# Performance work log

Measured on AMD Instinct MI355X. Metric: run time of the kernel, lower is better.

## Reference

```python
import jax, jax.numpy as jnp
import numpy as np

SAMPLE_RATE = 16000
FREQ_LOW = 200.0
FREQ_HIGH = 1200.0
# deterministic stand-in for random.uniform(freq_low, freq_high): midpoint
FREQUENCY = 0.5 * (FREQ_LOW + FREQ_HIGH)  # 700 Hz
CUTOFF = FREQUENCY / SAMPLE_RATE          # normalized cutoff, as in cutoff_frequency()
Q = 0.70710678  # standard Butterworth-like quality factor for biquad highpass


def _biquad_highpass_coeffs(cutoff, q):
    # standard audio-EQ-cookbook highpass biquad, cutoff normalized to sample rate
    w0 = 2.0 * np.pi * cutoff
    cw, sw = np.cos(w0), np.sin(w0)
    alpha = sw / (2.0 * q)
    b0 = (1.0 + cw) / 2.0
    b1 = -(1.0 + cw)
    b2 = (1.0 + cw) / 2.0
    a0 = 1.0 + alpha
    a1 = -2.0 * cw
    a2 = 1.0 - alpha
    return (np.float32(b0 / a0), np.float32(b1 / a0), np.float32(b2 / a0),
            np.float32(a1 / a0), np.float32(a2 / a0))


def setup_inputs() -> dict:
    key = jax.random.key(0)
    B, C, T = 128, 2, 65536
    audio = jax.random.normal(key, (B, C, T), dtype=jnp.float32)
    return {"audio": audio}


def reference(audio) -> jnp.ndarray:
    b0, b1, b2, a1, a2 = _biquad_highpass_coeffs(CUTOFF, Q)
    x_t = jnp.moveaxis(audio, -1, 0)  # [T, B, C] for scan over time
    zero = jnp.zeros(x_t.shape[1:], dtype=audio.dtype)

    def step(carry, x):
        x1, x2, y1, y2 = carry
        # IIR biquad difference equation
        y = b0 * x + b1 * x1 + b2 * x2 - a1 * y1 - a2 * y2
        return (x, x1, y, y1), y

    _, y_t = jax.lax.scan(step, (zero, zero, zero, zero), x_t)
    return jnp.moveaxis(y_t, 0, -1)  # [B, C, T]
```

## Files before the change

### kernel.cpp

```cpp
#include <hip/hip_runtime.h>
#include <math.h>


#define T_LEN    65536
#define L_CHUNK  64
#define W_WARM   64
#define TS       32
#define BLK      64
#define ROWS     64
#define BUF_F    (ROWS * TS)
#define BLOCKS_PER_CH 16

#define WAITVM(n) asm volatile("s_waitcnt vmcnt(" #n ")" ::: "memory")

__device__ __forceinline__ void lds_fence() {
    asm volatile("s_waitcnt lgkmcnt(0)" ::: "memory");
}

__device__ __forceinline__ void dma_tile(const float* __restrict__ x,
                                         int base_f, int tile, float* buf)
{
    #pragma unroll
    for (int i = 0; i < 8; ++i) {
        int pos = base_f + i * 512 + tile * TS;
        pos = pos < 0 ? 0 : pos;
        __builtin_amdgcn_global_load_lds(
            (__attribute__((address_space(1))) void*)(void*)(x + pos),
            (__attribute__((address_space(3))) void*)(buf + i * 256),
            16, 0, 0);
    }
}

template <bool WARM>
__device__ __forceinline__ void tile_filter(float* buf, int lane, bool ch0,
    float c_b0, float c_b1, float c_b2, float c_a1, float c_a2,
    float& x1, float& x2, float& y1, float& y2)
{
    float4 r[8];
    #pragma unroll
    for (int g = 0; g < 8; ++g)
        r[g] = *(float4*)&buf[(lane * 8 + ((g + lane) & 7)) * 4];

    if (WARM && ch0) {
        #pragma unroll
        for (int g = 0; g < 8; ++g) r[g] = make_float4(0.f, 0.f, 0.f, 0.f);
    }

    #pragma unroll
    for (int g = 0; g < 8; ++g) {
        float4 v = r[g];
        float yv;
        yv = c_b0*v.x + c_b1*x1 + c_b2*x2 - c_a1*y1 - c_a2*y2;
        x2 = x1; x1 = v.x; y2 = y1; y1 = yv; v.x = yv;
        yv = c_b0*v.y + c_b1*x1 + c_b2*x2 - c_a1*y1 - c_a2*y2;
        x2 = x1; x1 = v.y; y2 = y1; y1 = yv; v.y = yv;
        yv = c_b0*v.z + c_b1*x1 + c_b2*x2 - c_a1*y1 - c_a2*y2;
        x2 = x1; x1 = v.z; y2 = y1; y1 = yv; v.z = yv;
        yv = c_b0*v.w + c_b1*x1 + c_b2*x2 - c_a1*y1 - c_a2*y2;
        x2 = x1; x1 = v.w; y2 = y1; y1 = yv; v.w = yv;
        if (!WARM) r[g] = v;
    }

    if (!WARM) {
        #pragma unroll
        for (int g = 0; g < 8; ++g)
            *(float4*)&buf[(lane * 8 + ((g + lane) & 7)) * 4] = r[g];
    }
}

__global__ __launch_bounds__(BLK, 4)
void hp_biquad_kernel(const float* __restrict__ x, float* __restrict__ y,
                      float c_b0, float c_b1, float c_b2, float c_a1, float c_a2)
{
    __shared__ float bufA[BUF_F];
    __shared__ float bufB[BUF_F];
    const int lane = threadIdx.x;
    const int cg0  = blockIdx.x * ROWS;
    const bool ch0 = ((blockIdx.x & (BLOCKS_PER_CH - 1)) == 0) && (lane == 0);

    const int l0  = lane >> 3;
    const int j0  = ((lane & 7) - l0) & 7;
    const int bsf = (cg0 + l0) * L_CHUNK - W_WARM + j0 * 4;

    float x1 = 0.f, x2 = 0.f, y1 = 0.f, y2 = 0.f;

    dma_tile(x, bsf, 0, bufA);
    dma_tile(x, bsf, 1, bufB);

    WAITVM(8);
    tile_filter<true>(bufA, lane, ch0, c_b0, c_b1, c_b2, c_a1, c_a2, x1, x2, y1, y2);
    lds_fence();
    dma_tile(x, bsf, 2, bufA);

    WAITVM(8);
    tile_filter<true>(bufB, lane, ch0, c_b0, c_b1, c_b2, c_a1, c_a2, x1, x2, y1, y2);
    lds_fence();
    dma_tile(x, bsf, 3, bufB);

    WAITVM(8);
    tile_filter<false>(bufA, lane, ch0, c_b0, c_b1, c_b2, c_a1, c_a2, x1, x2, y1, y2);

    WAITVM(0);
    tile_filter<false>(bufB, lane, ch0, c_b0, c_b1, c_b2, c_a1, c_a2, x1, x2, y1, y2);
    lds_fence();

    const int ybase = cg0 * L_CHUNK + lane * 4;
    #pragma unroll
    for (int p = 0; p < 16; ++p) {
        int q   = lane + p * 64;
        int seg = q >> 4;
        int jj  = q & 15;
        float* b = (jj < 8) ? bufA : bufB;
        int g   = jj & 7;
        float4 v = *(float4*)&b[(seg * 8 + ((g + seg) & 7)) * 4];
        *(float4*)(y + ybase + p * 256) = v;
    }
}

extern "C" void kernel_launch(void* const* d_in, const int* in_sizes, int n_in,
                              void* d_out, int out_size, void* d_ws, size_t ws_size,
                              hipStream_t stream)
{
    const float* x = (const float*)d_in[0];
    float* y = (float*)d_out;

    const double SR = 16000.0, FLO = 200.0, FHI = 1200.0;
    const double freq   = 0.5 * (FLO + FHI);
    const double cutoff = freq / SR;
    const double q      = 0.70710678;
    const double w0 = 2.0 * M_PI * cutoff;
    const double cw = cos(w0), sw = sin(w0);
    const double alpha = sw / (2.0 * q);
    const double b0 = (1.0 + cw) / 2.0;
    const double b1 = -(1.0 + cw);
    const double b2 = (1.0 + cw) / 2.0;
    const double a0 = 1.0 + alpha;
    const double a1 = -2.0 * cw;
    const double a2 = 1.0 - alpha;
    const float fb0 = (float)(b0 / a0), fb1 = (float)(b1 / a0), fb2 = (float)(b2 / a0);
    const float fa1 = (float)(a1 / a0), fa2 = (float)(a2 / a0);

    const int total  = 128 * 2 * T_LEN;
    const int chunks = total / L_CHUNK;
    const int blocks = chunks / ROWS;

    hp_biquad_kernel<<<blocks, BLK, 0, stream>>>(x, y, fb0, fb1, fb2, fa1, fa2);
    (void)in_sizes; (void)n_in; (void)out_size; (void)d_ws; (void)ws_size;
}
```

Measured before the change: 114.9 us.

## Lengthen per-thread chunks to amortize IIR warm-up with a streaming tile loop

New measurement: 137.7 us. +19.8%, slower.

```diff
diff --git a/kernel.cpp b/kernel.cpp
--- a/kernel.cpp
+++ b/kernel.cpp
@@ -3,13 +3,15 @@
 
 
 #define T_LEN    65536
-#define L_CHUNK  64
+#define L_CHUNK  256
 #define W_WARM   64
 #define TS       32
 #define BLK      64
 #define ROWS     64
 #define BUF_F    (ROWS * TS)
-#define BLOCKS_PER_CH 16
+#define BLOCKS_PER_CH ((T_LEN / L_CHUNK) / ROWS)
+#define N_TILES  ((L_CHUNK + W_WARM) / TS)
+#define N_PAIRS  ((N_TILES - 2) / 2)
 
 #define WAITVM(n) asm volatile("s_waitcnt vmcnt(" #n ")" ::: "memory")
 
@@ -22,7 +24,7 @@
 {
     #pragma unroll
     for (int i = 0; i < 8; ++i) {
-        int pos = base_f + i * 512 + tile * TS;
+        int pos = base_f + i * (8 * L_CHUNK) + tile * TS;
         pos = pos < 0 ? 0 : pos;
         __builtin_amdgcn_global_load_lds(
             (__attribute__((address_space(1))) void*)(void*)(x + pos),
@@ -68,7 +70,7 @@
     }
 }
 
-__global__ __launch_bounds__(BLK, 4)
+__global__ __launch_bounds__(BLK, 2)
 void hp_biquad_kernel(const float* __restrict__ x, float* __restrict__ y,
                       float c_b0, float c_b1, float c_b2, float c_a1, float c_a2)
 {
@@ -97,23 +99,39 @@
     lds_fence();
     dma_tile(x, bsf, 3, bufB);
 
-    WAITVM(8);
-    tile_filter<false>(bufA, lane, ch0, c_b0, c_b1, c_b2, c_a1, c_a2, x1, x2, y1, y2);
+    const int ybase = cg0 * L_CHUNK;
+    #pragma unroll
+    for (int p = 0; p < N_PAIRS; ++p) {
+        if (p == 0) { WAITVM(8); } else { WAITVM(24); }
+        tile_filter<false>(bufA, lane, ch0, c_b0, c_b1, c_b2, c_a1, c_a2, x1, x2, y1, y2);
+        if (p == 0) { WAITVM(0); } else { WAITVM(16); }
+        tile_filter<false>(bufB, lane, ch0, c_b0, c_b1, c_b2, c_a1, c_a2, x1, x2, y1, y2);
+        lds_fence();
 
-    WAITVM(0);
-    tile_filter<false>(bufB, lane, ch0, c_b0, c_b1, c_b2, c_a1, c_a2, x1, x2, y1, y2);
-    lds_fence();
+        float4 v[16];
+        #pragma unroll
+        for (int k = 0; k < 16; ++k) {
+            int q  = lane + k * 64;
+            int sg = q >> 4;
+            int jj = q & 15;
+            float* b = (jj < 8) ? bufA : bufB;
+            int g  = jj & 7;
+            v[k] = *(float4*)&b[(sg * 8 + ((g + sg) & 7)) * 4];
+        }
+        lds_fence();
 
-    const int ybase = cg0 * L_CHUNK + lane * 4;
-    #pragma unroll
-    for (int p = 0; p < 16; ++p) {
-        int q   = lane + p * 64;
-        int seg = q >> 4;
-        int jj  = q & 15;
-        float* b = (jj < 8) ? bufA : bufB;
-        int g   = jj & 7;
-        float4 v = *(float4*)&b[(seg * 8 + ((g + seg) & 7)) * 4];
-        *(float4*)(y + ybase + p * 256) = v;
+        if (p < N_PAIRS - 1) {
+            dma_tile(x, bsf, 2 * p + 4, bufA);
+            dma_tile(x, bsf, 2 * p + 5, bufB);
+        }
+
+        #pragma unroll
+        for (int k = 0; k < 16; ++k) {
+            int q  = lane + k * 64;
+            int sg = q >> 4;
+            int jj = q & 15;
+            *(float4*)(y + ybase + sg * L_CHUNK + p * 64 + jj * 4) = v[k];
+        }
     }
 }
 
```

## Halve chunk length to double parallelism with six-tile warmup pipeline

Applied to the files above, without the earlier changes.

Result: slower. 237.8 us (+106.9%).

```diff
diff --git a/kernel.cpp b/kernel.cpp
--- a/kernel.cpp
+++ b/kernel.cpp
@@ -3,13 +3,14 @@
 
 
 #define T_LEN    65536
-#define L_CHUNK  64
+#define L_CHUNK  32
 #define W_WARM   64
-#define TS       32
+#define TS       16
 #define BLK      64
 #define ROWS     64
 #define BUF_F    (ROWS * TS)
-#define BLOCKS_PER_CH 16
+#define BLOCKS_PER_CH ((T_LEN / L_CHUNK) / ROWS)
+#define N_TILES  ((L_CHUNK + W_WARM) / TS)
 
 #define WAITVM(n) asm volatile("s_waitcnt vmcnt(" #n ")" ::: "memory")
 
@@ -21,7 +22,7 @@
                                          int base_f, int tile, float* buf)
 {
     #pragma unroll
-    for (int i = 0; i < 8; ++i) {
+    for (int i = 0; i < 4; ++i) {
         int pos = base_f + i * 512 + tile * TS;
         pos = pos < 0 ? 0 : pos;
         __builtin_amdgcn_global_load_lds(
@@ -32,22 +33,22 @@
 }
 
 template <bool WARM>
-__device__ __forceinline__ void tile_filter(float* buf, int lane, bool ch0,
+__device__ __forceinline__ void tile_filter(float* buf, int lane, bool zr,
     float c_b0, float c_b1, float c_b2, float c_a1, float c_a2,
     float& x1, float& x2, float& y1, float& y2)
 {
-    float4 r[8];
+    float4 r[4];
     #pragma unroll
-    for (int g = 0; g < 8; ++g)
-        r[g] = *(float4*)&buf[(lane * 8 + ((g + lane) & 7)) * 4];
+    for (int g = 0; g < 4; ++g)
+        r[g] = *(float4*)&buf[(lane * 4 + ((g + (lane >> 1)) & 3)) * 4];
 
-    if (WARM && ch0) {
+    if (WARM && zr) {
         #pragma unroll
-        for (int g = 0; g < 8; ++g) r[g] = make_float4(0.f, 0.f, 0.f, 0.f);
+        for (int g = 0; g < 4; ++g) r[g] = make_float4(0.f, 0.f, 0.f, 0.f);
     }
 
     #pragma unroll
-    for (int g = 0; g < 8; ++g) {
+    for (int g = 0; g < 4; ++g) {
         float4 v = r[g];
         float yv;
         yv = c_b0*v.x + c_b1*x1 + c_b2*x2 - c_a1*y1 - c_a2*y2;
@@ -63,12 +64,12 @@
 
     if (!WARM) {
         #pragma unroll
-        for (int g = 0; g < 8; ++g)
-            *(float4*)&buf[(lane * 8 + ((g + lane) & 7)) * 4] = r[g];
+        for (int g = 0; g < 4; ++g)
+            *(float4*)&buf[(lane * 4 + ((g + (lane >> 1)) & 3)) * 4] = r[g];
     }
 }
 
-__global__ __launch_bounds__(BLK, 4)
+__global__ __launch_bounds__(BLK, 5)
 void hp_biquad_kernel(const float* __restrict__ x, float* __restrict__ y,
                       float c_b0, float c_b1, float c_b2, float c_a1, float c_a2)
 {
@@ -76,44 +77,55 @@
     __shared__ float bufB[BUF_F];
     const int lane = threadIdx.x;
     const int cg0  = blockIdx.x * ROWS;
-    const bool ch0 = ((blockIdx.x & (BLOCKS_PER_CH - 1)) == 0) && (lane == 0);
+    const bool chf = (blockIdx.x & (BLOCKS_PER_CH - 1)) == 0;
 
-    const int l0  = lane >> 3;
-    const int j0  = ((lane & 7) - l0) & 7;
-    const int bsf = (cg0 + l0) * L_CHUNK - W_WARM + j0 * 4;
+    const int j0  = ((lane & 3) - (lane >> 3)) & 3;
+    const int bsf = (cg0 + (lane >> 2)) * L_CHUNK - W_WARM + j0 * 4;
 
     float x1 = 0.f, x2 = 0.f, y1 = 0.f, y2 = 0.f;
+
+    const bool zr01 = chf && (lane < 2);
+    const bool zr23 = chf && (lane == 0);
 
     dma_tile(x, bsf, 0, bufA);
     dma_tile(x, bsf, 1, bufB);
 
-    WAITVM(8);
-    tile_filter<true>(bufA, lane, ch0, c_b0, c_b1, c_b2, c_a1, c_a2, x1, x2, y1, y2);
+    WAITVM(4);
+    tile_filter<true>(bufA, lane, zr01, c_b0, c_b1, c_b2, c_a1, c_a2, x1, x2, y1, y2);
     lds_fence();
     dma_tile(x, bsf, 2, bufA);
 
-    WAITVM(8);
-    tile_filter<true>(bufB, lane, ch0, c_b0, c_b1, c_b2, c_a1, c_a2, x1, x2, y1, y2);
+    WAITVM(4);
+    tile_filter<true>(bufB, lane, zr01, c_b0, c_b1, c_b2, c_a1, c_a2, x1, x2, y1, y2);
     lds_fence();
     dma_tile(x, bsf, 3, bufB);
 
-    WAITVM(8);
-    tile_filter<false>(bufA, lane, ch0, c_b0, c_b1, c_b2, c_a1, c_a2, x1, x2, y1, y2);
+    WAITVM(4);
+    tile_filter<true>(bufA, lane, zr23, c_b0, c_b1, c_b2, c_a1, c_a2, x1, x2, y1, y2);
+    lds_fence();
+    dma_tile(x, bsf, 4, bufA);
+
+    WAITVM(4);
+    tile_filter<true>(bufB, lane, zr23, c_b0, c_b1, c_b2, c_a1, c_a2, x1, x2, y1, y2);
+    lds_fence();
+    dma_tile(x, bsf, 5, bufB);
+
+    WAITVM(4);
+    tile_filter<false>(bufA, lane, false, c_b0, c_b1, c_b2, c_a1, c_a2, x1, x2, y1, y2);
 
     WAITVM(0);
-    tile_filter<false>(bufB, lane, ch0, c_b0, c_b1, c_b2, c_a1, c_a2, x1, x2, y1, y2);
+    tile_filter<false>(bufB, lane, false, c_b0, c_b1, c_b2, c_a1, c_a2, x1, x2, y1, y2);
     lds_fence();
 
-    const int ybase = cg0 * L_CHUNK + lane * 4;
+    const int yb4 = cg0 * (L_CHUNK / 4);
     #pragma unroll
-    for (int p = 0; p < 16; ++p) {
-        int q   = lane + p * 64;
-        int seg = q >> 4;
-        int jj  = q & 15;
-        float* b = (jj < 8) ? bufA : bufB;
-        int g   = jj & 7;
-        float4 v = *(float4*)&b[(seg * 8 + ((g + seg) & 7)) * 4];
-        *(float4*)(y + ybase + p * 256) = v;
+    for (int k = 0; k < 8; ++k) {
+        int c  = k * 8 + (lane >> 3);
+        int jj = lane & 7;
+        float* b = (jj < 4) ? bufA : bufB;
+        int m  = ((jj & 3) + (c >> 1)) & 3;
+        float4 v = *(float4*)&b[(c * 4 + m) * 4];
+        *(float4*)(y + 4 * (yb4 + k * 64 + lane)) = v;
     }
 }
 
```

## Double chunk length so warm-up overhead shrinks, with 32 active rows per block

Applied to the files above, without the earlier changes.

Result: no change. 116.3 us (+1.2%).

```diff
diff --git a/kernel.cpp b/kernel.cpp
--- a/kernel.cpp
+++ b/kernel.cpp
@@ -3,13 +3,13 @@
 
 
 #define T_LEN    65536
-#define L_CHUNK  64
+#define L_CHUNK  128
 #define W_WARM   64
-#define TS       32
+#define TS       64
 #define BLK      64
-#define ROWS     64
+#define ROWS     32
 #define BUF_F    (ROWS * TS)
-#define BLOCKS_PER_CH 16
+#define BLOCKS_PER_CH ((T_LEN / L_CHUNK) / ROWS)
 
 #define WAITVM(n) asm volatile("s_waitcnt vmcnt(" #n ")" ::: "memory")
 
@@ -18,11 +18,11 @@
 }
 
 __device__ __forceinline__ void dma_tile(const float* __restrict__ x,
-                                         int base_f, int tile, float* buf)
+                                         int bE, int bO, int tile, float* buf)
 {
     #pragma unroll
     for (int i = 0; i < 8; ++i) {
-        int pos = base_f + i * 512 + tile * TS;
+        int pos = ((i & 1) ? bO : bE) + i * 512 + tile * TS;
         pos = pos < 0 ? 0 : pos;
         __builtin_amdgcn_global_load_lds(
             (__attribute__((address_space(1))) void*)(void*)(x + pos),
@@ -32,23 +32,23 @@
 }
 
 template <bool WARM>
-__device__ __forceinline__ void tile_filter(float* buf, int lane, bool ch0,
+__device__ __forceinline__ void tile_filter(float* buf, int l, bool zr,
     float c_b0, float c_b1, float c_b2, float c_a1, float c_a2,
     float& x1, float& x2, float& y1, float& y2)
 {
-    float4 r[8];
+    float4 r[16];
     #pragma unroll
-    for (int g = 0; g < 8; ++g)
-        r[g] = *(float4*)&buf[(lane * 8 + ((g + lane) & 7)) * 4];
+    for (int j = 0; j < 16; ++j)
+        r[j] = *(float4*)&buf[(l * 16 + ((j + (l & 7)) & 15)) * 4];
 
-    if (WARM && ch0) {
+    if (WARM && zr) {
         #pragma unroll
-        for (int g = 0; g < 8; ++g) r[g] = make_float4(0.f, 0.f, 0.f, 0.f);
+        for (int j = 0; j < 16; ++j) r[j] = make_float4(0.f, 0.f, 0.f, 0.f);
     }
 
     #pragma unroll
-    for (int g = 0; g < 8; ++g) {
-        float4 v = r[g];
+    for (int j = 0; j < 16; ++j) {
+        float4 v = r[j];
         float yv;
         yv = c_b0*v.x + c_b1*x1 + c_b2*x2 - c_a1*y1 - c_a2*y2;
         x2 = x1; x1 = v.x; y2 = y1; y1 = yv; v.x = yv;
@@ -58,13 +58,13 @@
         x2 = x1; x1 = v.z; y2 = y1; y1 = yv; v.z = yv;
         yv = c_b0*v.w + c_b1*x1 + c_b2*x2 - c_a1*y1 - c_a2*y2;
         x2 = x1; x1 = v.w; y2 = y1; y1 = yv; v.w = yv;
-        if (!WARM) r[g] = v;
+        if (!WARM) r[j] = v;
     }
 
     if (!WARM) {
         #pragma unroll
-        for (int g = 0; g < 8; ++g)
-            *(float4*)&buf[(lane * 8 + ((g + lane) & 7)) * 4] = r[g];
+        for (int j = 0; j < 16; ++j)
+            *(float4*)&buf[(l * 16 + ((j + (l & 7)) & 15)) * 4] = r[j];
     }
 }
 
@@ -76,44 +76,47 @@
     __shared__ float bufB[BUF_F];
     const int lane = threadIdx.x;
     const int cg0  = blockIdx.x * ROWS;
-    const bool ch0 = ((blockIdx.x & (BLOCKS_PER_CH - 1)) == 0) && (lane == 0);
+    const bool chf = (blockIdx.x & (BLOCKS_PER_CH - 1)) == 0;
+    const bool zr  = chf && (lane == 0);
 
-    const int l0  = lane >> 3;
-    const int j0  = ((lane & 7) - l0) & 7;
-    const int bsf = (cg0 + l0) * L_CHUNK - W_WARM + j0 * 4;
+    const int rq = lane >> 4;
+    const int m  = lane & 15;
+    const int jE = (m - rq) & 15;
+    const int jO = (m - rq - 4) & 15;
+    const int rowbase = (cg0 + rq) * L_CHUNK - W_WARM;
+    const int bE = rowbase + jE * 4;
+    const int bO = rowbase + jO * 4;
 
     float x1 = 0.f, x2 = 0.f, y1 = 0.f, y2 = 0.f;
 
-    dma_tile(x, bsf, 0, bufA);
-    dma_tile(x, bsf, 1, bufB);
+    dma_tile(x, bE, bO, 0, bufA);
+    dma_tile(x, bE, bO, 1, bufB);
 
     WAITVM(8);
-    tile_filter<true>(bufA, lane, ch0, c_b0, c_b1, c_b2, c_a1, c_a2, x1, x2, y1, y2);
+    if (lane < ROWS)
+        tile_filter<true>(bufA, lane, zr, c_b0, c_b1, c_b2, c_a1, c_a2, x1, x2, y1, y2);
     lds_fence();
-    dma_tile(x, bsf, 2, bufA);
+    dma_tile(x, bE, bO, 2, bufA);
 
     WAITVM(8);
-    tile_filter<true>(bufB, lane, ch0, c_b0, c_b1, c_b2, c_a1, c_a2, x1, x2, y1, y2);
-    lds_fence();
-    dma_tile(x, bsf, 3, bufB);
-
-    WAITVM(8);
-    tile_filter<false>(bufA, lane, ch0, c_b0, c_b1, c_b2, c_a1, c_a2, x1, x2, y1, y2);
+    if (lane < ROWS)
+        tile_filter<false>(bufB, lane, false, c_b0, c_b1, c_b2, c_a1, c_a2, x1, x2, y1, y2);
 
     WAITVM(0);
-    tile_filter<false>(bufB, lane, ch0, c_b0, c_b1, c_b2, c_a1, c_a2, x1, x2, y1, y2);
+    if (lane < ROWS)
+        tile_filter<false>(bufA, lane, false, c_b0, c_b1, c_b2, c_a1, c_a2, x1, x2, y1, y2);
     lds_fence();
 
-    const int ybase = cg0 * L_CHUNK + lane * 4;
+    const int yb4 = cg0 * (L_CHUNK / 4);
     #pragma unroll
-    for (int p = 0; p < 16; ++p) {
-        int q   = lane + p * 64;
-        int seg = q >> 4;
-        int jj  = q & 15;
-        float* b = (jj < 8) ? bufA : bufB;
-        int g   = jj & 7;
-        float4 v = *(float4*)&b[(seg * 8 + ((g + seg) & 7)) * 4];
-        *(float4*)(y + ybase + p * 256) = v;
+    for (int k = 0; k < 16; ++k) {
+        int q  = k * 64 + lane;
+        int c  = q >> 5;
+        int w  = q & 31;
+        float* b = (w < 16) ? bufB : bufA;
+        int mm = ((w & 15) + (c & 7)) & 15;
+        float4 v = *(float4*)&b[(c * 16 + mm) * 4];
+        *(float4*)(y + 4 * (yb4 + q)) = v;
     }
 }
 
```
